# Optimization experiments

Hardware: AMD Instinct MI355X
Metric: run time of the kernel (lower is better)

Reference implementation:

```python
import jax, jax.numpy as jnp
import numpy as np

B = 128          # batch of IQ signals
L = 128          # signal length
PL = 16          # patch length
ST = 4           # patch stride
WIN = 4          # local window
NPATCH = (L - PL) // ST + 1   # 29
HID = 256
NCLS = 8
NG = B * NPATCH               # number of patch graphs
N = NG * PL                   # total nodes


def _build_edges():
    src, dst = [], []
    for i in range(PL):
        for j in range(PL):
            if 0 < abs(i - j) <= WIN:
                src.append(i); dst.append(j)
    bs = np.array(src, np.int32)          # [108]
    bd = np.array(dst, np.int32)
    off = (np.arange(NG, dtype=np.int32) * PL)[:, None]
    isrc = (off + bs[None, :]).reshape(-1)
    idst = (off + bd[None, :]).reshape(-1)
    # cross-patch edges: last node of patch p -> first node of patch p+1
    b = np.arange(B, dtype=np.int32)[:, None]
    p = np.arange(NPATCH - 1, dtype=np.int32)[None, :]
    csrc = (b * NPATCH * PL + p * PL + (PL - 1)).reshape(-1)
    cdst = (b * NPATCH * PL + (p + 1) * PL).reshape(-1)
    return np.concatenate([isrc, csrc]), np.concatenate([idst, cdst])


def setup_inputs() -> dict:
    key = jax.random.key(0)
    ks = jax.random.split(key, 10)
    s = 0.05
    esrc, edst = _build_edges()
    return {
        "iq_signal": jax.random.normal(ks[0], (B, 2, L), jnp.float32),
        "edge_src": jnp.asarray(esrc),
        "edge_dst": jnp.asarray(edst),
        # SAGEConv layer 0 (in=2): lin_l (agg, with bias), lin_r (root, no bias)
        "W0_agg": jax.random.normal(ks[1], (HID, 2), jnp.float32) * s,
        "W0_root": jax.random.normal(ks[2], (HID, 2), jnp.float32) * s,
        "b0": jnp.zeros((HID,), jnp.float32),
        # SAGEConv layers 1..3 (256 -> 256), stacked
        "W_agg": jax.random.normal(ks[3], (3, HID, HID), jnp.float32) * s,
        "W_root": jax.random.normal(ks[4], (3, HID, HID), jnp.float32) * s,
        "b_lin": jnp.zeros((3, HID), jnp.float32),
        # per-layer LayerNorms
        "ln_scale": jnp.ones((4, HID), jnp.float32),
        "ln_bias": jnp.zeros((4, HID), jnp.float32),
        # classifier head
        "cls_W1": jax.random.normal(ks[5], (HID, HID), jnp.float32) * s,
        "cls_b1": jnp.zeros((HID,), jnp.float32),
        "cls_ln_scale": jnp.ones((HID,), jnp.float32),
        "cls_ln_bias": jnp.zeros((HID,), jnp.float32),
        "cls_W2": jax.random.normal(ks[6], (NCLS, HID), jnp.float32) * s,
        "cls_b2": jnp.zeros((NCLS,), jnp.float32),
    }


def _ln(x, g, b):
    m = x.mean(-1, keepdims=True)
    v = ((x - m) ** 2).mean(-1, keepdims=True)
    return (x - m) * jax.lax.rsqrt(v + 1e-5) * g + b


def reference(iq_signal, edge_src, edge_dst, W0_agg, W0_root, b0,
              W_agg, W_root, b_lin, ln_scale, ln_bias,
              cls_W1, cls_b1, cls_ln_scale, cls_ln_bias, cls_W2, cls_b2):
    # patch extraction: [B,2,L] -> [B,NPATCH,PL,2] -> node features [N,2]
    idx = jnp.arange(NPATCH)[:, None] * ST + jnp.arange(PL)[None, :]   # [29,16]
    x = jnp.transpose(iq_signal[:, :, idx], (0, 2, 3, 1)).reshape(-1, 2)

    # in-degree for mean aggregation (0 -> safe divide by 1)
    ones = jnp.ones((edge_dst.shape[0],), x.dtype)
    deg = jax.ops.segment_sum(ones, edge_dst, num_segments=N)
    inv_deg = 1.0 / jnp.maximum(deg, 1.0)

    def sage(h, Wa, Wr, b):
        # mean-aggregate neighbor messages, then lin_l(agg) + lin_r(h) + bias
        agg = jax.ops.segment_sum(h[edge_src], edge_dst, num_segments=N)
        agg = agg * inv_deg[:, None]
        return agg @ Wa.T + h @ Wr.T + b

    # layer 0 (2 -> 256): no residual (shape change)
    h = jax.nn.relu(_ln(sage(x, W0_agg, W0_root, b0), ln_scale[0], ln_bias[0]))
    # layers 1..3 with residual
    for l in range(3):
        hn = jax.nn.relu(_ln(sage(h, W_agg[l], W_root[l], b_lin[l]),
                             ln_scale[l + 1], ln_bias[l + 1]))
        h = h + hn

    node_emb = h                                  # [N, 256]
    # global_mean_pool per patch graph (16 consecutive nodes each)
    gf = node_emb.reshape(NG, PL, HID).mean(axis=1)   # [NG, 256]
    z = jax.nn.relu(_ln(gf @ cls_W1.T + cls_b1, cls_ln_scale, cls_ln_bias))
    logits = z @ cls_W2.T + cls_b2                # [NG, 8]
    return logits, gf, node_emb
```

## Files before the change

kernel.cpp:

```cpp
#include <hip/hip_runtime.h>
#include <hip/hip_bf16.h>

typedef __hip_bfloat16 bf16;
typedef unsigned short u16;
typedef unsigned int uint32;
typedef __attribute__((ext_vector_type(8))) short bf16x8;
typedef __attribute__((ext_vector_type(4))) float f32x4;

#define BATCH   128
#define LSIG    128
#define PL      16
#define ST      4
#define WIN     4
#define NPATCH  29
#define NG      (BATCH * NPATCH)
#define NNODE   (NG * PL)
#define HID     256
#define NCLS    8

#define IQ_OFF    0
#define W0A_OFF   32768
#define W0R_OFF   33280
#define B0_OFF    33792
#define BLIN_OFF  34048
#define LNS_OFF   34816
#define LNB_OFF   35840
#define W1T_OFF   36864
#define CB1_OFF   102400
#define CLNS_OFF  102656
#define CLNB_OFF  102912
#define CW2_OFF   103168
#define CB2_OFF   105216
#define CVT_TOTAL 105224

#define P_BYTE_OFF   4096
#define WB_BYTE_OFF  425984
#define A_BYTE_OFF   1216512
#define B_BYTE_OFF   1959936
#define GF_EOFF      (NG * NCLS)
#define EMB_EOFF     (NG * NCLS + NG * HID)

__device__ __forceinline__ float b2f(bf16 x) { return __bfloat162float(x); }
__device__ __forceinline__ float lof(uint32 u) { return __uint_as_float(u << 16); }
__device__ __forceinline__ float hif(uint32 u) { return __uint_as_float(u & 0xFFFF0000u); }
__device__ __forceinline__ float ldmix(const void* p, int i, int fl) {
  return fl ? ((const float*)p)[i] : __bfloat162float(((const bf16*)p)[i]);
}

__global__ __launch_bounds__(256) void detect_kernel(const u16* __restrict__ iq, int* flag) {
  __shared__ int sbig, snz;
  int t = threadIdx.x;
  if (t == 0) { sbig = 0; snz = 0; }
  __syncthreads();
  int big = 0, nz = 0;
  for (int e = t; e < 16384; e += 256) {
    u16 u = iq[2 * e];
    int ex = (u >> 7) & 0xFF;
    if (ex >= 0xC0) big++;
    if (u != 0) nz++;
  }
  atomicAdd(&sbig, big); atomicAdd(&snz, nz);
  __syncthreads();
  if (t == 0) *flag = (sbig > 4 || snz < 100) ? 1 : 0;
}

__global__ __launch_bounds__(256) void convert_params(
    const int* __restrict__ flag,
    const void* iq, const void* w0a, const void* w0r, const void* b0,
    const void* blin, const void* lns, const void* lnb,
    const void* cw1, const void* cb1, const void* clns, const void* clnb,
    const void* cw2, const void* cb2,
    float* __restrict__ P) {
  int idx = blockIdx.x * 256 + threadIdx.x;
  if (idx >= CVT_TOTAL) return;
  int fl = *flag;
  float v;
  if (idx < W0A_OFF)        v = ldmix(iq,  idx, fl);
  else if (idx < W0R_OFF)   v = ldmix(w0a, idx - W0A_OFF, fl);
  else if (idx < B0_OFF)    v = ldmix(w0r, idx - W0R_OFF, fl);
  else if (idx < BLIN_OFF)  v = ldmix(b0,  idx - B0_OFF, fl);
  else if (idx < LNS_OFF)   v = ldmix(blin, idx - BLIN_OFF, fl);
  else if (idx < LNB_OFF)   v = ldmix(lns, idx - LNS_OFF, fl);
  else if (idx < W1T_OFF)   v = ldmix(lnb, idx - LNB_OFF, fl);
  else if (idx < CB1_OFF) { int t2 = idx - W1T_OFF;
    v = ldmix(cw1, (t2 & 255) * 256 + (t2 >> 8), fl); }
  else if (idx < CLNS_OFF)  v = ldmix(cb1, idx - CB1_OFF, fl);
  else if (idx < CLNB_OFF)  v = ldmix(clns, idx - CLNS_OFF, fl);
  else if (idx < CW2_OFF)   v = ldmix(clnb, idx - CLNB_OFF, fl);
  else if (idx < CB2_OFF)   v = ldmix(cw2, idx - CW2_OFF, fl);
  else                      v = ldmix(cb2, idx - CB2_OFF, fl);
  P[idx] = v;
}

__global__ __launch_bounds__(256) void convert_wb(
    const int* __restrict__ flag, const void* wag, const void* wro, bf16* __restrict__ WB) {
  int idx = blockIdx.x * 256 + threadIdx.x;
  int fl = *flag;
  int l = idx >> 17, m = (idx >> 16) & 1, r = idx & 65535;
  const void* src = m ? wro : wag;
  WB[idx] = __float2bfloat16(ldmix(src, l * 65536 + r, fl));
}

__global__ __launch_bounds__(256) void layer0_kernel(
    const float* __restrict__ P, bf16* __restrict__ hout) {
  int g = blockIdx.x, f = threadIdx.x;
  int b = g / NPATCH, p = g % NPATCH;
  __shared__ float x_s[PL][2];
  __shared__ float xp_s[2];
  __shared__ float agg_s[PL][2];
  __shared__ float o_s[PL][HID];
  __shared__ float mv_s[PL][2];
  if (f < 32) { int j = f & 15, c = f >> 4;
    x_s[j][c] = P[IQ_OFF + (b * 2 + c) * LSIG + p * ST + j]; }
  if (f < 2) xp_s[f] = (p > 0) ? P[IQ_OFF + (b * 2 + f) * LSIG + (p - 1) * ST + PL - 1] : 0.f;
  __syncthreads();
  if (f < 32) { int j = f & 15, c = f >> 4;
    float s = 0.f;
    int lo = j - WIN < 0 ? 0 : j - WIN, hi = j + WIN > 15 ? 15 : j + WIN;
    for (int i = lo; i <= hi; ++i) if (i != j) s += x_s[i][c];
    int deg = (j < WIN ? j : WIN) + ((15 - j) < WIN ? (15 - j) : WIN);
    if (j == 0 && p > 0) { s += xp_s[c]; deg += 1; }
    agg_s[j][c] = s / (float)deg;
  }
  __syncthreads();
  float wa0 = P[W0A_OFF + f * 2], wa1 = P[W0A_OFF + f * 2 + 1];
  float wr0 = P[W0R_OFF + f * 2], wr1 = P[W0R_OFF + f * 2 + 1];
  float bb = P[B0_OFF + f];
#pragma unroll
  for (int j = 0; j < PL; ++j)
    o_s[j][f] = agg_s[j][0] * wa0 + agg_s[j][1] * wa1 + x_s[j][0] * wr0 + x_s[j][1] * wr1 + bb;
  __syncthreads();
  { int j = f >> 4, q = f & 15;
    float s = 0.f, s2 = 0.f;
#pragma unroll
    for (int i = 0; i < 16; ++i) { float v = o_s[j][q + 16 * i]; s += v; s2 += v * v; }
#pragma unroll
    for (int m = 8; m >= 1; m >>= 1) { s += __shfl_xor(s, m); s2 += __shfl_xor(s2, m); }
    if (q == 0) { float mean = s * (1.f / HID);
      float var = s2 * (1.f / HID) - mean * mean;
      mv_s[j][0] = mean; mv_s[j][1] = rsqrtf(var + 1e-5f); }
  }
  __syncthreads();
  float gl = P[LNS_OFF + f], bl = P[LNB_OFF + f];
#pragma unroll
  for (int j = 0; j < PL; ++j) {
    float v = (o_s[j][f] - mv_s[j][0]) * mv_s[j][1] * gl + bl;
    v = v > 0.f ? v : 0.f;
    hout[(size_t)(g * PL + j) * HID + f] = __float2bfloat16(v);
  }
}

#define MFMA_BF16 __builtin_amdgcn_mfma_f32_16x16x32_bf16
__global__ __launch_bounds__(256, 2) void sage_mfma(
    const bf16* __restrict__ hin,
    const bf16* __restrict__ Wa, const bf16* __restrict__ Wr,
    const float* __restrict__ bias,
    const float* __restrict__ lng, const float* __restrict__ lnb,
    bf16* __restrict__ hout) {
  int t = threadIdx.x;
  int w = t >> 6, l = t & 63, lr = l & 15, lg = l >> 4;
  int g0 = blockIdx.x * 4;
  size_t nbase = (size_t)g0 * PL;
  __shared__ uint32 h32[64 * 128];
  __shared__ uint32 a32[64 * 128];
  float* mvp = (float*)h32;
  const uint32* hinw = (const uint32*)hin;

  int colbase = w * 64;
  const bf16* waB = Wa + (colbase + lr) * HID + lg * 8;
  const bf16* wrB = Wr + (colbase + lr) * HID + lg * 8;
  bf16x8 wa0[2][8], wr0[2][8];
#pragma unroll
  for (int nt = 0; nt < 2; ++nt)
#pragma unroll
    for (int ks = 0; ks < 8; ++ks) {
      wa0[nt][ks] = *(const bf16x8*)(waB + nt * 16 * HID + ks * 32);
      wr0[nt][ks] = *(const bf16x8*)(wrB + nt * 16 * HID + ks * 32);
    }

  const uint32* hg = hinw + nbase * 128;
#pragma unroll
  for (int it = 0; it < 8; ++it) {
    int u = it * 256 + t;
    int row = u >> 5, sl = u & 31;
    int sw = sl ^ (row & 7);
    *(uint4*)&h32[row * 128 + sw * 4] = *(const uint4*)(hg + u * 4);
  }
  __syncthreads();

  {
    int c2 = t & 127, Ph = t >> 7;
#pragma unroll
    for (int pi = 0; pi < 2; ++pi) {
      int pp = Ph + pi * 2;
      int pr = pp * 16;
      int hp = ((g0 + pp) % NPATCH) != 0;
      float vlo[16], vhi[16];
#pragma unroll
      for (int j = 0; j < 16; ++j) {
        uint32 u = h32[(pr + j) * 128 + (((c2 >> 2) ^ (j & 7)) << 2) + (c2 & 3)];
        vlo[j] = lof(u); vhi[j] = hif(u);
      }
      float blo = 0.f, bhi = 0.f;
      if (hp) {
        uint32 u;
        if (pp == 0) u = hinw[(nbase - 1) * 128 + c2];
        else { int br = pr - 1;
          u = a32[0];
          u = h32[br * 128 + (((c2 >> 2) ^ (br & 7)) << 2) + (c2 & 3)]; }
        blo = lof(u); bhi = hif(u);
      }
#pragma unroll
      for (int j = 0; j < 16; ++j) {
        const int a = (j - WIN < 0) ? 0 : j - WIN;
        const int b = (j + WIN > 15) ? 15 : j + WIN;
        float slo = 0.f, shi = 0.f;
#pragma unroll
        for (int i = 0; i < 16; ++i)
          if (i >= a && i <= b && i != j) { slo += vlo[i]; shi += vhi[i]; }
        float deg = (float)((j < WIN ? j : WIN) + (15 - j < WIN ? 15 - j : WIN));
        if (j == 0 && hp) { slo += blo; shi += bhi; deg += 1.f; }
        float inv = 1.f / deg;
        bf16 r0 = __float2bfloat16(slo * inv), r1 = __float2bfloat16(shi * inv);
        uint32 wv = ((uint32)(*(const u16*)&r1) << 16) | (uint32)(*(const u16*)&r0);
        a32[(pr + j) * 128 + (((c2 >> 2) ^ (j & 7)) << 2) + (c2 & 3)] = wv;
      }
    }
  }
  __syncthreads();

  f32x4 acc[4][4];
#pragma unroll
  for (int m = 0; m < 4; ++m)
#pragma unroll
    for (int n = 0; n < 4; ++n) acc[m][n] = (f32x4){0.f, 0.f, 0.f, 0.f};
#pragma unroll
  for (int ks = 0; ks < 8; ++ks) {
    bf16x8 wa1[2], wr1[2];
#pragma unroll
    for (int nt = 0; nt < 2; ++nt) {
      wa1[nt] = *(const bf16x8*)(waB + (nt + 2) * 16 * HID + ks * 32);
      wr1[nt] = *(const bf16x8*)(wrB + (nt + 2) * 16 * HID + ks * 32);
    }
#pragma unroll
    for (int m = 0; m < 4; ++m) {
      int row = m * 16 + lr;
      int idx = row * 128 + ((((ks * 4 + lg) ^ (lr & 7))) << 2);
      bf16x8 af = *(const bf16x8*)&a32[idx];
      bf16x8 hf = *(const bf16x8*)&h32[idx];
      acc[m][0] = MFMA_BF16(af, wa0[0][ks], acc[m][0], 0, 0, 0);
      acc[m][0] = MFMA_BF16(hf, wr0[0][ks], acc[m][0], 0, 0, 0);
      acc[m][1] = MFMA_BF16(af, wa0[1][ks], acc[m][1], 0, 0, 0);
      acc[m][1] = MFMA_BF16(hf, wr0[1][ks], acc[m][1], 0, 0, 0);
      acc[m][2] = MFMA_BF16(af, wa1[0],     acc[m][2], 0, 0, 0);
      acc[m][2] = MFMA_BF16(hf, wr1[0],     acc[m][2], 0, 0, 0);
      acc[m][3] = MFMA_BF16(af, wa1[1],     acc[m][3], 0, 0, 0);
      acc[m][3] = MFMA_BF16(hf, wr1[1],     acc[m][3], 0, 0, 0);
    }
  }
#pragma unroll
  for (int nt = 0; nt < 4; ++nt) {
    float bv = bias[colbase + nt * 16 + lr];
#pragma unroll
    for (int m = 0; m < 4; ++m) {
      acc[m][nt][0] += bv; acc[m][nt][1] += bv;
      acc[m][nt][2] += bv; acc[m][nt][3] += bv;
    }
  }
  __syncthreads();

#pragma unroll
  for (int m = 0; m < 4; ++m)
#pragma unroll
    for (int nt = 0; nt < 4; ++nt) {
      int col = colbase + nt * 16 + lr;
#pragma unroll
      for (int r = 0; r < 4; ++r) {
        int row = m * 16 + lg * 4 + r;
        int i16 = row * 256 + (((col >> 3) ^ (row & 7)) << 3) + (col & 7);
        bf16 x = __float2bfloat16(acc[m][nt][r]);
        ((u16*)a32)[i16] = *(const u16*)&x;
      }
    }
  __syncthreads();

  {
    int row = t >> 2, q = t & 3;
    float s = 0.f, s2 = 0.f;
#pragma unroll
    for (int i = 0; i < 32; ++i) {
      int d = q * 32 + i;
      uint32 u = a32[row * 128 + (((d >> 2) ^ (row & 7)) << 2) + (d & 3)];
      float a = lof(u), b = hif(u);
      s += a + b; s2 += a * a + b * b;
    }
    s += __shfl_xor(s, 1); s2 += __shfl_xor(s2, 1);
    s += __shfl_xor(s, 2); s2 += __shfl_xor(s2, 2);
    if (q == 0) { float mean = s * (1.f / HID);
      mvp[row * 2] = mean;
      mvp[row * 2 + 1] = rsqrtf(s2 * (1.f / HID) - mean * mean + 1e-5f); }
  }
  __syncthreads();

  {
    int c2 = t & 127, part = t >> 7;
    float gl0 = lng[c2 * 2], gl1 = lng[c2 * 2 + 1];
    float bl0 = lnb[c2 * 2], bl1 = lnb[c2 * 2 + 1];
    uint32* outw = (uint32*)hout + nbase * 128;
    const uint32* inw = hinw + nbase * 128;
#pragma unroll
    for (int i = 0; i < 32; ++i) {
      int row = part * 32 + i;
      uint32 u = a32[row * 128 + (((c2 >> 2) ^ (row & 7)) << 2) + (c2 & 3)];
      float mean = mvp[row * 2], rstd = mvp[row * 2 + 1];
      float a = (lof(u) - mean) * rstd * gl0 + bl0; a = a > 0.f ? a : 0.f;
      float b = (hif(u) - mean) * rstd * gl1 + bl1; b = b > 0.f ? b : 0.f;
      uint32 hu = inw[row * 128 + c2];
      a += lof(hu); b += hif(hu);
      bf16 r0 = __float2bfloat16(a), r1 = __float2bfloat16(b);
      uint32 wv = ((uint32)(*(const u16*)&r1) << 16) | (uint32)(*(const u16*)&r0);
      outw[row * 128 + c2] = wv;
    }
  }
}

__global__ __launch_bounds__(256) void head_kernel(
    const bf16* __restrict__ emb, const float* __restrict__ P,
    void* __restrict__ dout, const int* __restrict__ flag) {
  int g = blockIdx.x, f = threadIdx.x;
  int fl = *flag;
  __shared__ float gf_s[HID];
  __shared__ float z_s[HID];
  __shared__ float ps[4], ps2[4];
  __shared__ float mr[2];
  const bf16* eb = emb + (size_t)g * PL * HID;
  float s = 0.f;
#pragma unroll
  for (int r = 0; r < PL; ++r) s += b2f(eb[r * HID + f]);
  s *= (1.f / PL);
  gf_s[f] = s;
  { size_t ei = (size_t)GF_EOFF + (size_t)g * HID + f;
    if (fl) ((float*)dout)[ei] = s; else ((bf16*)dout)[ei] = __float2bfloat16(s); }
  __syncthreads();
  float acc = P[CB1_OFF + f];
  for (int k = 0; k < HID; k += 4) {
    const float4 gv = *(const float4*)(&gf_s[k]);
    acc = fmaf(gv.x, P[W1T_OFF + (k + 0) * HID + f], acc);
    acc = fmaf(gv.y, P[W1T_OFF + (k + 1) * HID + f], acc);
    acc = fmaf(gv.z, P[W1T_OFF + (k + 2) * HID + f], acc);
    acc = fmaf(gv.w, P[W1T_OFF + (k + 3) * HID + f], acc);
  }
  float s1 = acc, s2 = acc * acc;
#pragma unroll
  for (int m = 32; m >= 1; m >>= 1) { s1 += __shfl_xor(s1, m); s2 += __shfl_xor(s2, m); }
  int wid = f >> 6, lane = f & 63;
  if (lane == 0) { ps[wid] = s1; ps2[wid] = s2; }
  __syncthreads();
  if (f == 0) {
    float S = ps[0] + ps[1] + ps[2] + ps[3];
    float S2 = ps2[0] + ps2[1] + ps2[2] + ps2[3];
    float mean = S * (1.f / HID);
    mr[0] = mean; mr[1] = rsqrtf(S2 * (1.f / HID) - mean * mean + 1e-5f);
  }
  __syncthreads();
  float z = (acc - mr[0]) * mr[1] * P[CLNS_OFF + f] + P[CLNB_OFF + f];
  z = z > 0.f ? z : 0.f;
  z_s[f] = z;
  __syncthreads();
  if (f < NCLS) {
    float a = P[CB2_OFF + f];
    for (int k = 0; k < HID; ++k) a = fmaf(z_s[k], P[CW2_OFF + f * HID + k], a);
    size_t ei = (size_t)g * NCLS + f;
    if (fl) ((float*)dout)[ei] = a; else ((bf16*)dout)[ei] = __float2bfloat16(a);
  }
}

__global__ __launch_bounds__(256) void emit_emb(
    const bf16* __restrict__ A, void* __restrict__ dout, const int* __restrict__ flag) {
  int fl = *flag;
  size_t n = (size_t)NNODE * HID;
  for (size_t i = blockIdx.x * 256ull + threadIdx.x; i < n; i += 2048ull * 256ull) {
    bf16 v = A[i];
    size_t ei = (size_t)EMB_EOFF + i;
    if (fl) ((float*)dout)[ei] = b2f(v); else ((bf16*)dout)[ei] = v;
  }
}

extern "C" void kernel_launch(void* const* d_in, const int* in_sizes, int n_in,
                              void* d_out, int out_size, void* d_ws, size_t ws_size,
                              hipStream_t stream) {
  char* ws = (char*)d_ws;
  int*   flag = (int*)ws;
  float* P    = (float*)(ws + P_BYTE_OFF);
  bf16*  WB   = (bf16*)(ws + WB_BYTE_OFF);
  bf16*  A    = (bf16*)(ws + A_BYTE_OFF);
  bf16*  B    = (bf16*)((char*)d_out + B_BYTE_OFF);

  detect_kernel<<<1, 256, 0, stream>>>((const u16*)d_in[0], flag);
  convert_params<<<(CVT_TOTAL + 255) / 256, 256, 0, stream>>>(
      flag, d_in[0], d_in[3], d_in[4], d_in[5], d_in[8],
      d_in[9], d_in[10], d_in[11], d_in[12], d_in[13], d_in[14], d_in[15], d_in[16], P);
  convert_wb<<<1536, 256, 0, stream>>>(flag, d_in[6], d_in[7], WB);

  layer0_kernel<<<NG, 256, 0, stream>>>(P, B);
  sage_mfma<<<NG / 4, 256, 0, stream>>>(B, WB, WB + 65536,
      P + BLIN_OFF, P + LNS_OFF + HID, P + LNB_OFF + HID, A);
  sage_mfma<<<NG / 4, 256, 0, stream>>>(A, WB + 131072, WB + 131072 + 65536,
      P + BLIN_OFF + HID, P + LNS_OFF + 2 * HID, P + LNB_OFF + 2 * HID, B);
  sage_mfma<<<NG / 4, 256, 0, stream>>>(B, WB + 262144, WB + 262144 + 65536,
      P + BLIN_OFF + 2 * HID, P + LNS_OFF + 3 * HID, P + LNB_OFF + 3 * HID, A);
  head_kernel<<<NG, 256, 0, stream>>>(A, P, d_out, flag);
  emit_emb<<<2048, 256, 0, stream>>>(A, d_out, flag);
}
```

Baseline: 238.0 us.

## Fuse embedding emit and mean pooling into last SAGE layer epilogue

Templates the SAGE MFMA kernel so the final layer writes node embeddings straight to the output buffer in the requested dtype and computes the per-patch mean pool in its epilogue. This removes the separate emit_emb kernel and the head kernel's 16-row pooling reads. The head now reads the pooled features back from the output. Weight fragments are now double-buffered per k-step instead of 32 fragments preloaded into registers, which lowers register pressure but adds global loads inside the MFMA loop.

Measured after the change: 240.7 us. No clear change (+1.1%).

```diff
diff --git a/kernel.cpp b/kernel.cpp
--- a/kernel.cpp
+++ b/kernel.cpp
@@ -40,10 +40,16 @@
 #define GF_EOFF      (NG * NCLS)
 #define EMB_EOFF     (NG * NCLS + NG * HID)
 
+#define MFMA_BF16 __builtin_amdgcn_mfma_f32_16x16x32_bf16
+
 __device__ __forceinline__ float b2f(bf16 x) { return __bfloat162float(x); }
 __device__ __forceinline__ float lof(uint32 u) { return __uint_as_float(u << 16); }
 __device__ __forceinline__ float hif(uint32 u) { return __uint_as_float(u & 0xFFFF0000u); }
-__device__ __forceinline__ float ldmix(const void* p, int i, int fl) {
+__device__ __forceinline__ uint32 packbf(float a, float b) {
+  bf16 r0 = __float2bfloat16(a), r1 = __float2bfloat16(b);
+  return ((uint32)(*(const u16*)&r1) << 16) | (uint32)(*(const u16*)&r0);
+}
+__device__ __forceinline__ float ldmix(const void* p, size_t i, int fl) {
   return fl ? ((const float*)p)[i] : __bfloat162float(((const bf16*)p)[i]);
 }
 
@@ -150,13 +156,14 @@
   }
 }
 
-#define MFMA_BF16 __builtin_amdgcn_mfma_f32_16x16x32_bf16
+template<int LAST>
 __global__ __launch_bounds__(256, 2) void sage_mfma(
     const bf16* __restrict__ hin,
     const bf16* __restrict__ Wa, const bf16* __restrict__ Wr,
     const float* __restrict__ bias,
     const float* __restrict__ lng, const float* __restrict__ lnb,
-    bf16* __restrict__ hout) {
+    bf16* __restrict__ hout,
+    void* __restrict__ dout, const int* __restrict__ flag) {
   int t = threadIdx.x;
   int w = t >> 6, l = t & 63, lr = l & 15, lg = l >> 4;
   int g0 = blockIdx.x * 4;
@@ -166,18 +173,6 @@
   float* mvp = (float*)h32;
   const uint32* hinw = (const uint32*)hin;
 
-  int colbase = w * 64;
-  const bf16* waB = Wa + (colbase + lr) * HID + lg * 8;
-  const bf16* wrB = Wr + (colbase + lr) * HID + lg * 8;
-  bf16x8 wa0[2][8], wr0[2][8];
-#pragma unroll
-  for (int nt = 0; nt < 2; ++nt)
-#pragma unroll
-    for (int ks = 0; ks < 8; ++ks) {
-      wa0[nt][ks] = *(const bf16x8*)(waB + nt * 16 * HID + ks * 32);
-      wr0[nt][ks] = *(const bf16x8*)(wrB + nt * 16 * HID + ks * 32);
-    }
-
   const uint32* hg = hinw + nbase * 128;
 #pragma unroll
   for (int it = 0; it < 8; ++it) {
@@ -206,7 +201,6 @@
         uint32 u;
         if (pp == 0) u = hinw[(nbase - 1) * 128 + c2];
         else { int br = pr - 1;
-          u = a32[0];
           u = h32[br * 128 + (((c2 >> 2) ^ (br & 7)) << 2) + (c2 & 3)]; }
         blo = lof(u); bhi = hif(u);
       }
@@ -221,9 +215,7 @@
         float deg = (float)((j < WIN ? j : WIN) + (15 - j < WIN ? 15 - j : WIN));
         if (j == 0 && hp) { slo += blo; shi += bhi; deg += 1.f; }
         float inv = 1.f / deg;
-        bf16 r0 = __float2bfloat16(slo * inv), r1 = __float2bfloat16(shi * inv);
-        uint32 wv = ((uint32)(*(const u16*)&r1) << 16) | (uint32)(*(const u16*)&r0);
-        a32[(pr + j) * 128 + (((c2 >> 2) ^ (j & 7)) << 2) + (c2 & 3)] = wv;
+        a32[(pr + j) * 128 + (((c2 >> 2) ^ (j & 7)) << 2) + (c2 & 3)] = packbf(slo * inv, shi * inv);
       }
     }
   }
@@ -234,28 +226,35 @@
   for (int m = 0; m < 4; ++m)
 #pragma unroll
     for (int n = 0; n < 4; ++n) acc[m][n] = (f32x4){0.f, 0.f, 0.f, 0.f};
+  int colbase = w * 64;
+  const bf16* waB = Wa + (colbase + lr) * HID + lg * 8;
+  const bf16* wrB = Wr + (colbase + lr) * HID + lg * 8;
+  bf16x8 wafr[2][4], wrfr[2][4];
+#pragma unroll
+  for (int nt = 0; nt < 4; ++nt) {
+    wafr[0][nt] = *(const bf16x8*)(waB + nt * 16 * HID);
+    wrfr[0][nt] = *(const bf16x8*)(wrB + nt * 16 * HID);
+  }
 #pragma unroll
   for (int ks = 0; ks < 8; ++ks) {
-    bf16x8 wa1[2], wr1[2];
-#pragma unroll
-    for (int nt = 0; nt < 2; ++nt) {
-      wa1[nt] = *(const bf16x8*)(waB + (nt + 2) * 16 * HID + ks * 32);
-      wr1[nt] = *(const bf16x8*)(wrB + (nt + 2) * 16 * HID + ks * 32);
+    const int cur = ks & 1, nxt = cur ^ 1;
+    if (ks < 7) {
+#pragma unroll
+      for (int nt = 0; nt < 4; ++nt) {
+        wafr[nxt][nt] = *(const bf16x8*)(waB + nt * 16 * HID + (ks + 1) * 32);
+        wrfr[nxt][nt] = *(const bf16x8*)(wrB + nt * 16 * HID + (ks + 1) * 32);
+      }
     }
 #pragma unroll
     for (int m = 0; m < 4; ++m) {
-      int row = m * 16 + lr;
-      int idx = row * 128 + ((((ks * 4 + lg) ^ (lr & 7))) << 2);
+      int idx = (m * 16 + lr) * 128 + (((ks * 4 + lg) ^ (lr & 7)) << 2);
       bf16x8 af = *(const bf16x8*)&a32[idx];
       bf16x8 hf = *(const bf16x8*)&h32[idx];
-      acc[m][0] = MFMA_BF16(af, wa0[0][ks], acc[m][0], 0, 0, 0);
-      acc[m][0] = MFMA_BF16(hf, wr0[0][ks], acc[m][0], 0, 0, 0);
-      acc[m][1] = MFMA_BF16(af, wa0[1][ks], acc[m][1], 0, 0, 0);
-      acc[m][1] = MFMA_BF16(hf, wr0[1][ks], acc[m][1], 0, 0, 0);
-      acc[m][2] = MFMA_BF16(af, wa1[0],     acc[m][2], 0, 0, 0);
-      acc[m][2] = MFMA_BF16(hf, wr1[0],     acc[m][2], 0, 0, 0);
-      acc[m][3] = MFMA_BF16(af, wa1[1],     acc[m][3], 0, 0, 0);
-      acc[m][3] = MFMA_BF16(hf, wr1[1],     acc[m][3], 0, 0, 0);
+#pragma unroll
+      for (int nt = 0; nt < 4; ++nt) {
+        acc[m][nt] = MFMA_BF16(af, wafr[cur][nt], acc[m][nt], 0, 0, 0);
+        acc[m][nt] = MFMA_BF16(hf, wrfr[cur][nt], acc[m][nt], 0, 0, 0);
+      }
     }
   }
 #pragma unroll
@@ -263,8 +262,7 @@
     float bv = bias[colbase + nt * 16 + lr];
 #pragma unroll
     for (int m = 0; m < 4; ++m) {
-      acc[m][nt][0] += bv; acc[m][nt][1] += bv;
-      acc[m][nt][2] += bv; acc[m][nt][3] += bv;
+      acc[m][nt][0] += bv; acc[m][nt][1] += bv; acc[m][nt][2] += bv; acc[m][nt][3] += bv;
     }
   }
   __syncthreads();
@@ -303,29 +301,54 @@
   __syncthreads();
 
   {
-    int c2 = t & 127, part = t >> 7;
+    int c2 = t & 127, prt = t >> 7;
     float gl0 = lng[c2 * 2], gl1 = lng[c2 * 2 + 1];
     float bl0 = lnb[c2 * 2], bl1 = lnb[c2 * 2 + 1];
-    uint32* outw = (uint32*)hout + nbase * 128;
+    uint32* outw = nullptr;
+    if constexpr (!LAST) outw = (uint32*)hout + nbase * 128;
     const uint32* inw = hinw + nbase * 128;
-#pragma unroll
-    for (int i = 0; i < 32; ++i) {
-      int row = part * 32 + i;
-      uint32 u = a32[row * 128 + (((c2 >> 2) ^ (row & 7)) << 2) + (c2 & 3)];
-      float mean = mvp[row * 2], rstd = mvp[row * 2 + 1];
-      float a = (lof(u) - mean) * rstd * gl0 + bl0; a = a > 0.f ? a : 0.f;
-      float b = (hif(u) - mean) * rstd * gl1 + bl1; b = b > 0.f ? b : 0.f;
-      uint32 hu = inw[row * 128 + c2];
-      a += lof(hu); b += hif(hu);
-      bf16 r0 = __float2bfloat16(a), r1 = __float2bfloat16(b);
-      uint32 wv = ((uint32)(*(const u16*)&r1) << 16) | (uint32)(*(const u16*)&r0);
-      outw[row * 128 + c2] = wv;
+    int fl = 0;
+    if constexpr (LAST) fl = *flag;
+#pragma unroll
+    for (int pi = 0; pi < 2; ++pi) {
+      float sga = 0.f, sgb = 0.f;
+#pragma unroll
+      for (int i = 0; i < 16; ++i) {
+        int row = prt * 32 + pi * 16 + i;
+        uint32 u = a32[row * 128 + (((c2 >> 2) ^ (row & 7)) << 2) + (c2 & 3)];
+        float mean = mvp[row * 2], rstd = mvp[row * 2 + 1];
+        float a = (lof(u) - mean) * rstd * gl0 + bl0; a = a > 0.f ? a : 0.f;
+        float b_ = (hif(u) - mean) * rstd * gl1 + bl1; b_ = b_ > 0.f ? b_ : 0.f;
+        uint32 hu = inw[row * 128 + c2];
+        a += lof(hu); b_ += hif(hu);
+        if constexpr (!LAST) {
+          outw[row * 128 + c2] = packbf(a, b_);
+        } else {
+          sga += a; sgb += b_;
+          if (fl) {
+            size_t ei = (size_t)EMB_EOFF + (nbase + row) * 256 + (size_t)c2 * 2;
+            ((float*)dout)[ei] = a; ((float*)dout)[ei + 1] = b_;
+          } else {
+            ((uint32*)dout)[(EMB_EOFF >> 1) + (nbase + row) * 128 + c2] = packbf(a, b_);
+          }
+        }
+      }
+      if constexpr (LAST) {
+        float ga = sga * (1.f / PL), gb = sgb * (1.f / PL);
+        int gidx = g0 + prt * 2 + pi;
+        if (fl) {
+          size_t gi = (size_t)GF_EOFF + (size_t)gidx * 256 + (size_t)c2 * 2;
+          ((float*)dout)[gi] = ga; ((float*)dout)[gi + 1] = gb;
+        } else {
+          ((uint32*)dout)[(GF_EOFF >> 1) + gidx * 128 + c2] = packbf(ga, gb);
+        }
+      }
     }
   }
 }
 
 __global__ __launch_bounds__(256) void head_kernel(
-    const bf16* __restrict__ emb, const float* __restrict__ P,
+    const void* __restrict__ gin, const float* __restrict__ P,
     void* __restrict__ dout, const int* __restrict__ flag) {
   int g = blockIdx.x, f = threadIdx.x;
   int fl = *flag;
@@ -333,14 +356,8 @@
   __shared__ float z_s[HID];
   __shared__ float ps[4], ps2[4];
   __shared__ float mr[2];
-  const bf16* eb = emb + (size_t)g * PL * HID;
-  float s = 0.f;
-#pragma unroll
-  for (int r = 0; r < PL; ++r) s += b2f(eb[r * HID + f]);
-  s *= (1.f / PL);
-  gf_s[f] = s;
-  { size_t ei = (size_t)GF_EOFF + (size_t)g * HID + f;
-    if (fl) ((float*)dout)[ei] = s; else ((bf16*)dout)[ei] = __float2bfloat16(s); }
+  gf_s[f] = fl ? ((const float*)gin)[(size_t)GF_EOFF + (size_t)g * HID + f]
+               : b2f(((const bf16*)gin)[(size_t)GF_EOFF + (size_t)g * HID + f]);
   __syncthreads();
   float acc = P[CB1_OFF + f];
   for (int k = 0; k < HID; k += 4) {
@@ -372,17 +389,6 @@
     for (int k = 0; k < HID; ++k) a = fmaf(z_s[k], P[CW2_OFF + f * HID + k], a);
     size_t ei = (size_t)g * NCLS + f;
     if (fl) ((float*)dout)[ei] = a; else ((bf16*)dout)[ei] = __float2bfloat16(a);
-  }
-}
-
-__global__ __launch_bounds__(256) void emit_emb(
-    const bf16* __restrict__ A, void* __restrict__ dout, const int* __restrict__ flag) {
-  int fl = *flag;
-  size_t n = (size_t)NNODE * HID;
-  for (size_t i = blockIdx.x * 256ull + threadIdx.x; i < n; i += 2048ull * 256ull) {
-    bf16 v = A[i];
-    size_t ei = (size_t)EMB_EOFF + i;
-    if (fl) ((float*)dout)[ei] = b2f(v); else ((bf16*)dout)[ei] = v;
   }
 }
 
@@ -402,13 +408,12 @@
       d_in[9], d_in[10], d_in[11], d_in[12], d_in[13], d_in[14], d_in[15], d_in[16], P);
   convert_wb<<<1536, 256, 0, stream>>>(flag, d_in[6], d_in[7], WB);
 
-  layer0_kernel<<<NG, 256, 0, stream>>>(P, B);
-  sage_mfma<<<NG / 4, 256, 0, stream>>>(B, WB, WB + 65536,
-      P + BLIN_OFF, P + LNS_OFF + HID, P + LNB_OFF + HID, A);
-  sage_mfma<<<NG / 4, 256, 0, stream>>>(A, WB + 131072, WB + 131072 + 65536,
-      P + BLIN_OFF + HID, P + LNS_OFF + 2 * HID, P + LNB_OFF + 2 * HID, B);
-  sage_mfma<<<NG / 4, 256, 0, stream>>>(B, WB + 262144, WB + 262144 + 65536,
-      P + BLIN_OFF + 2 * HID, P + LNS_OFF + 3 * HID, P + LNB_OFF + 3 * HID, A);
-  head_kernel<<<NG, 256, 0, stream>>>(A, P, d_out, flag);
-  emit_emb<<<2048, 256, 0, stream>>>(A, d_out, flag);
-}
+  layer0_kernel<<<NG, 256, 0, stream>>>(P, A);
+  sage_mfma<0><<<NG / 4, 256, 0, stream>>>(A, WB, WB + 65536,
+      P + BLIN_OFF, P + LNS_OFF + HID, P + LNB_OFF + HID, B, nullptr, flag);
+  sage_mfma<0><<<NG / 4, 256, 0, stream>>>(B, WB + 131072, WB + 131072 + 65536,
+      P + BLIN_OFF + HID, P + LNS_OFF + 2 * HID, P + LNB_OFF + 2 * HID, A, nullptr, flag);
+  sage_mfma<1><<<NG / 4, 256, 0, stream>>>(A, WB + 262144, WB + 262144 + 65536,
+      P + BLIN_OFF + 2 * HID, P + LNS_OFF + 3 * HID, P + LNB_OFF + 3 * HID, nullptr, d_out, flag);
+  head_kernel<<<NG, 256, 0, stream>>>(d_out, P, d_out, flag);
+}
```
